# Optimization experiments

Hardware: AMD Instinct MI355X
Metric: run time of the kernel (lower is better)

The kernel has to match this reference:

```python
import jax, jax.numpy as jnp
import numpy as np

N = 20000      # nodes
E = 160000     # edges
F_IN = 128     # num_node_features
D = 128        # embedding_size (out_channels)
H = 4          # heads
NEG = 0.2      # GATv2Conv negative_slope
N_LAYERS = 3


def setup_inputs() -> dict:
    key = jax.random.key(0)
    ks = jax.random.split(key, 12)
    s = 0.05
    return {
        "x": jax.random.normal(ks[0], (N, F_IN), jnp.float32),
        "edge_index": jax.random.randint(ks[1], (2, E), 0, N, jnp.int64),
        "edge_attr": jax.random.normal(ks[2], (E, 2), jnp.float32),
        "Wf": jax.random.normal(ks[3], (F_IN, D), jnp.float32) * s,
        "bf": jnp.zeros((D,), jnp.float32),
        "Wl": jax.random.normal(ks[4], (D, H * D), jnp.float32) * s,
        "bl": jnp.zeros((H * D,), jnp.float32),
        "Wr": jax.random.normal(ks[5], (D, H * D), jnp.float32) * s,
        "br": jnp.zeros((H * D,), jnp.float32),
        "We": jax.random.normal(ks[6], (2, H * D), jnp.float32) * s,
        "att": jax.random.normal(ks[7], (H, D), jnp.float32) * s,
        "bias_out": jnp.zeros((D,), jnp.float32),
    }


def reference(x, edge_index, edge_attr, Wf, bf, Wl, bl, Wr, br, We, att, bias_out):
    src, dst = edge_index[0], edge_index[1]

    # add_self_loops with fill_value='mean': self-loop edge_attr = mean of
    # incoming edge_attr per node (0 where a node has no incoming edges)
    ea_sum = jax.ops.segment_sum(edge_attr, dst, num_segments=N)            # [N,2]
    cnt = jax.ops.segment_sum(jnp.ones((E,), edge_attr.dtype), dst, num_segments=N)
    loop_attr = ea_sum / jnp.maximum(cnt, 1.0)[:, None]
    loop_idx = jnp.arange(N, dtype=src.dtype)
    fsrc = jnp.concatenate([src, loop_idx])                                  # [E+N]
    fdst = jnp.concatenate([dst, loop_idx])
    fea = jnp.concatenate([edge_attr, loop_attr], axis=0)                    # [E+N,2]

    ee = (fea @ We).reshape(-1, H, D)                                        # [E+N,H,D]

    def gatv2_layer(h):
        xl = (h @ Wl + bl).reshape(N, H, D)   # lin_l -> source-side / message
        xr = (h @ Wr + br).reshape(N, H, D)   # lin_r -> target-side
        e = jax.nn.leaky_relu(xl[fsrc] + xr[fdst] + ee, NEG)                 # [E+N,H,D]
        logits = jnp.einsum('ehd,hd->eh', e, att)                            # [E+N,H]
        m = jax.ops.segment_max(logits, fdst, num_segments=N)                # [N,H]
        w = jnp.exp(logits - m[fdst])
        denom = jax.ops.segment_sum(w, fdst, num_segments=N)                 # [N,H]
        alpha = w / denom[fdst]                                              # segment softmax
        msg = xl[fsrc] * alpha[..., None]                                    # [E+N,H,D]
        out = jax.ops.segment_sum(msg, fdst, num_segments=N)                 # [N,H,D]
        return out.mean(axis=1) + bias_out                                   # concat=False

    h = x @ Wf + bf
    for _ in range(N_LAYERS):
        h = jax.nn.leaky_relu(gatv2_layer(h), 0.01)  # F.leaky_relu default slope
    return h
```

## Files before the change

kernel.cpp:

```cpp
#include <hip/hip_runtime.h>
#include <hip/hip_bf16.h>

#define NN 20000
#define NE 160000
#define EF (NE + NN)
#define DD 128
#define HH 4
#define NPA (NN * DD)
#define NPW (1024 * 128 + 128 * 128 + 1024)
#define DEGB ((NE + 255) / 256)
#define NBLK 40

typedef unsigned short u16;
typedef unsigned int u32;

using short8  = __attribute__((ext_vector_type(8))) short;
using ushort8 = __attribute__((ext_vector_type(8))) unsigned short;
using float4v = __attribute__((ext_vector_type(4))) float;
using f32x2   = __attribute__((ext_vector_type(2))) float;

__device__ __forceinline__ float bf2f(u16 u) {
    union { u32 i; float f; } c;
    c.i = ((u32)u) << 16;
    return c.f;
}
__device__ __forceinline__ u16 f2bf(float f) {
    union { float f; u32 u; } c;
    c.f = f;
    u32 u = c.u;
    u32 r = (u + 0x7fffu + ((u >> 16) & 1u)) >> 16;
    return (u16)r;
}

template<int CTRL>
__device__ __forceinline__ float dpp_add(float v) {
    int t = __builtin_amdgcn_update_dpp(0, __builtin_bit_cast(int, v),
                                        CTRL, 0xf, 0xf, true);
    return v + __builtin_bit_cast(float, t);
}


__global__ void k_zero_i(int* __restrict__ p, int n) {
    int i = blockIdx.x * blockDim.x + threadIdx.x;
    if (i < n) p[i] = 0;
}

__global__ void k_zero_f(float* __restrict__ p, int n) {
    int i = blockIdx.x * blockDim.x + threadIdx.x;
    if (i < n) p[i] = 0.f;
}


__global__ void k_degpack(const int* __restrict__ ei, const float* __restrict__ ea,
                          const float* __restrict__ x,
                          const float* __restrict__ Wl, const float* __restrict__ Wr,
                          const float* __restrict__ bl, const float* __restrict__ br,
                          const float* __restrict__ Wf,
                          int* __restrict__ cnt, float* __restrict__ ea_sum,
                          u16* __restrict__ Axh, u16* __restrict__ Axl,
                          u16* __restrict__ W2Th, u16* __restrict__ W2Tl,
                          u16* __restrict__ WfTh, u16* __restrict__ WfTl,
                          float* __restrict__ bias2) {
    int gb = blockIdx.x;
    if (gb < DEGB) {
        int e = gb * 256 + threadIdx.x;
        if (e >= NE) return;
        int t = ei[NE + e];
        atomicAdd(&cnt[t], 1);
        atomicAdd(&ea_sum[t * 2 + 0], ea[e * 2 + 0]);
        atomicAdd(&ea_sum[t * 2 + 1], ea[e * 2 + 1]);
        return;
    }
    int i = (gb - DEGB) * 256 + threadIdx.x;
    if (i < NPA) {
        float a = x[i];
        u16 h = f2bf(a);
        Axh[i] = h;
        Axl[i] = f2bf(a - bf2f(h));
        return;
    }
    i -= NPA;
    if (i < 1024 * 128) {
        int n = i >> 7, k = i & 127;
        float w = (n < 512) ? Wl[k * 512 + n] : Wr[k * 512 + (n - 512)];
        u16 h = f2bf(w);
        W2Th[n * 128 + k] = h;
        W2Tl[n * 128 + k] = f2bf(w - bf2f(h));
    } else if (i < 1024 * 128 + 128 * 128) {
        int u = i - 1024 * 128;
        int n = u >> 7, k = u & 127;
        float w = Wf[k * 128 + n];
        u16 h = f2bf(w);
        WfTh[n * 128 + k] = h;
        WfTl[n * 128 + k] = f2bf(w - bf2f(h));
    } else if (i < NPW) {
        int n = i - (1024 * 128 + 128 * 128);
        bias2[n] = (n < 512) ? bl[n] : br[n - 512];
    }
}


__global__ __launch_bounds__(512) void k_scan_a(const int* __restrict__ cnt,
                                                int* __restrict__ rowptr,
                                                int* __restrict__ bsum) {
    __shared__ int ws[8];
    int tid = threadIdx.x;
    int i = blockIdx.x * 512 + tid;
    int l = tid & 63, w = tid >> 6;
    int v = (i < NN) ? (cnt[i] + 1) : 0;
    #pragma unroll
    for (int off = 1; off < 64; off <<= 1) {
        int u = __shfl_up(v, off, 64);
        if (l >= off) v += u;
    }
    if (l == 63) ws[w] = v;
    __syncthreads();
    if (w == 0) {
        int s = (l < 8) ? ws[l] : 0;
        #pragma unroll
        for (int off = 1; off < 8; off <<= 1) {
            int u = __shfl_up(s, off, 64);
            if (l >= off) s += u;
        }
        if (l < 8) ws[l] = s;
    }
    __syncthreads();
    v += (w > 0) ? ws[w - 1] : 0;
    if (i < NN) rowptr[i + 1] = v;
    if (tid == 511) bsum[blockIdx.x] = v;
}

__global__ void k_scan_c(int* __restrict__ rowptr, const int* __restrict__ bsum) {
    int l = threadIdx.x & 63;
    int v = (l < NBLK) ? bsum[l] : 0;
    #pragma unroll
    for (int off = 1; off < 64; off <<= 1) {
        int u = __shfl_up(v, off, 64);
        if (l >= off) v += u;
    }
    int i = blockIdx.x * blockDim.x + threadIdx.x;
    int j = i >> 9;
    int off = (j > 0) ? __shfl(v, j - 1, 64) : 0;
    if (i < NN) rowptr[i + 1] += off;
    if (i == 0) rowptr[0] = 0;
}


__global__ void k_fill(const int* __restrict__ ei, const float* __restrict__ ea,
                       const int* __restrict__ rowptr, int* __restrict__ fillc,
                       const int* __restrict__ cnt, const float* __restrict__ ea_sum,
                       int* __restrict__ srcs,
                       float* __restrict__ fa0, float* __restrict__ fa1) {
    int e = blockIdx.x * blockDim.x + threadIdx.x;
    if (e < NE) {
        int s = ei[e], t = ei[NE + e];
        int pos = atomicAdd(&fillc[t], 1);
        int slot = rowptr[t] + pos;
        srcs[slot] = s;
        fa0[slot] = ea[e * 2];
        fa1[slot] = ea[e * 2 + 1];
    } else if (e < NE + NN) {
        int n = e - NE;
        int slot = rowptr[n + 1] - 1;
        srcs[slot] = n;
        float c = fmaxf((float)cnt[n], 1.f);
        fa0[slot] = ea_sum[n * 2 + 0] / c;
        fa1[slot] = ea_sum[n * 2 + 1] / c;
    }
}


template<int SPLIT, int NB>
__global__ __launch_bounds__(256, 3) void k_mgemm(
        const u16* __restrict__ Ahg, const u16* __restrict__ Alg,
        const u16* __restrict__ BTh, const u16* __restrict__ BTl,
        const float* __restrict__ bias, float* __restrict__ C1,
        u16* __restrict__ C2b,
        u16* __restrict__ Oh, u16* __restrict__ Ol, int M) {
    __shared__ u16 sAh[64 * 128], sBh[64 * 128], sBl[64 * 128];
    int m0 = blockIdx.y * 64;
    int t = threadIdx.x;
    int lane = t & 63;
    int wm = (t >> 6) & 1;
    int wn = t >> 7;
    int fm = lane & 15;
    int q8 = (lane >> 4) * 8;

    short8 fal[4][2];
    #pragma unroll
    for (int i = 0; i < 2; ++i) {
        const u16* p = Alg + (size_t)(m0 + wm * 32 + i * 16 + fm) * 128 + q8;
        #pragma unroll
        for (int kk = 0; kk < 4; ++kk)
            fal[kk][i] = *(const short8*)(p + kk * 32);
    }

    #pragma unroll
    for (int i = 0; i < 4; ++i) {
        int c = t + 256 * i;
        int row = c >> 4, ch = c & 15;
        int gm = m0 + row;
        short8 va = {0, 0, 0, 0, 0, 0, 0, 0};
        if (gm < M) va = *(const short8*)&Ahg[gm * 128 + ch * 8];
        *(short8*)&sAh[row * 128 + ((ch ^ (row & 15)) << 3)] = va;
    }

    int cq = q8 >> 3;

    for (int bb = 0; bb < NB; ++bb) {
        int n0 = (blockIdx.x * NB + bb) * 64;
        __syncthreads();
        #pragma unroll
        for (int i = 0; i < 4; ++i) {
            int c = t + 256 * i;
            int row = c >> 4, ch = c & 15;
            int gn = n0 + row;
            int d = row * 128 + ((ch ^ (row & 15)) << 3);
            *(short8*)&sBh[d] = *(const short8*)&BTh[gn * 128 + ch * 8];
            *(short8*)&sBl[d] = *(const short8*)&BTl[gn * 128 + ch * 8];
        }
        __syncthreads();

        float4v zz = {0.f, 0.f, 0.f, 0.f};
        float4v acc[2][2];
        acc[0][0] = zz; acc[0][1] = zz; acc[1][0] = zz; acc[1][1] = zz;

        #pragma unroll
        for (int k0 = 0; k0 < 128; k0 += 32) {
            int cl = (k0 >> 3) + cq;
            int sw = (cl ^ fm) << 3;
            short8 fah[2], fbh[2], fbl[2];
            #pragma unroll
            for (int i = 0; i < 2; ++i) {
                int mr = wm * 32 + i * 16 + fm;
                fah[i] = *(const short8*)&sAh[mr * 128 + sw];
                int nr = wn * 32 + i * 16 + fm;
                fbh[i] = *(const short8*)&sBh[nr * 128 + sw];
                fbl[i] = *(const short8*)&sBl[nr * 128 + sw];
            }
            #pragma unroll
            for (int i = 0; i < 2; ++i)
                #pragma unroll
                for (int j = 0; j < 2; ++j) {
                    acc[i][j] = __builtin_amdgcn_mfma_f32_16x16x32_bf16(fah[i], fbh[j], acc[i][j], 0, 0, 0);
                    acc[i][j] = __builtin_amdgcn_mfma_f32_16x16x32_bf16(fah[i], fbl[j], acc[i][j], 0, 0, 0);
                    acc[i][j] = __builtin_amdgcn_mfma_f32_16x16x32_bf16(fal[k0 >> 5][i], fbh[j], acc[i][j], 0, 0, 0);
                }
        }

        #pragma unroll
        for (int i = 0; i < 2; ++i) {
            #pragma unroll
            for (int j = 0; j < 2; ++j) {
                int gn = n0 + wn * 32 + j * 16 + fm;
                float bv = bias[gn];
                #pragma unroll
                for (int r = 0; r < 4; ++r) {
                    int gm = m0 + wm * 32 + i * 16 + (lane >> 4) * 4 + r;
                    if (gm < M) {
                        float v = acc[i][j][r] + bv;
                        if (SPLIT) {
                            u16 h = f2bf(v);
                            Oh[gm * 128 + gn] = h;
                            Ol[gm * 128 + gn] = f2bf(v - bf2f(h));
                        } else if (n0 < 512) {
                            C1[gm * 512 + gn] = v;
                        } else {
                            C2b[gm * 512 + gn - 512] = f2bf(v);
                        }
                    }
                }
            }
        }
    }
}


__global__ __launch_bounds__(256) void k_gat(
        const int* __restrict__ rowptr, const int* __restrict__ srcs,
        const float* __restrict__ fa0, const float* __restrict__ fa1,
        const float* __restrict__ xl, const u16* __restrict__ xr,
        const float* __restrict__ We, const float* __restrict__ att,
        const float* __restrict__ bias_out,
        u16* __restrict__ Oh, u16* __restrict__ Ol,
        float* __restrict__ outp, int last) {
    __shared__ float sacc[2][512];
    __shared__ float sden[2][4];
    int wv = threadIdx.x >> 6;
    int pair = wv >> 1;
    int half = wv & 1;
    int n = blockIdx.x * 2 + pair;
    int l = threadIdx.x & 63;
    int d0 = l * 8;

    f32x2 xr2[4], we0p[4], we1p[4], at6p[4], at4p[4];
    {
        ushort8 u = *reinterpret_cast<const ushort8*>(&xr[(size_t)n * 512 + d0]);
        #pragma unroll
        for (int k = 0; k < 4; ++k) {
            f32x2 t; t.x = bf2f(u[2 * k]); t.y = bf2f(u[2 * k + 1]);
            xr2[k] = t;
        }
        const f32x2* w0 = reinterpret_cast<const f32x2*>(&We[d0]);
        const f32x2* w1 = reinterpret_cast<const f32x2*>(&We[512 + d0]);
        const f32x2* av = reinterpret_cast<const f32x2*>(&att[d0]);
        #pragma unroll
        for (int k = 0; k < 4; ++k) {
            we0p[k] = w0[k];
            we1p[k] = w1[k];
            f32x2 a = av[k];
            at6p[k] = a * 0.6f;
            at4p[k] = a * 0.4f;
        }
    }

    int b0 = rowptr[n], b1 = rowptr[n + 1];
    int nit = (b1 - b0 - half + 1) >> 1;

    int sv = 0, f0i = 0, f1i = 0;
    {
        int me = b0 + half + 2 * l;
        if (l < nit) {
            sv  = srcs[me];
            f0i = __builtin_bit_cast(int, fa0[me]);
            f1i = __builtin_bit_cast(int, fa1[me]);
        }
    }

    f32x2 acc2[4];
    acc2[0] = f32x2{0.f, 0.f}; acc2[1] = f32x2{0.f, 0.f};
    acc2[2] = f32x2{0.f, 0.f}; acc2[3] = f32x2{0.f, 0.f};
    float den = 0.f;

    auto body = [&](float4 A, float4 B, float f0, float f1) {
        f32x2 f0p; f0p.x = f0; f0p.y = f0;
        f32x2 f1p; f1p.x = f1; f1p.y = f1;
        f32x2 xv2[4];
        xv2[0].x = A.x; xv2[0].y = A.y;
        xv2[1].x = A.z; xv2[1].y = A.w;
        xv2[2].x = B.x; xv2[2].y = B.y;
        xv2[3].x = B.z; xv2[3].y = B.w;
        f32x2 p2 = {0.f, 0.f};
        #pragma unroll
        for (int k = 0; k < 4; ++k) {
            f32x2 t = __builtin_elementwise_fma(f0p, we0p[k], xr2[k]);
            t = __builtin_elementwise_fma(f1p, we1p[k], t);
            f32x2 v2 = xv2[k] + t;
            f32x2 a2 = __builtin_elementwise_abs(v2);
            p2 = __builtin_elementwise_fma(at6p[k], v2, p2);
            p2 = __builtin_elementwise_fma(at4p[k], a2, p2);
        }
        float p = p2.x + p2.y;
        p = dpp_add<0xB1>(p);
        p = dpp_add<0x4E>(p);
        p = dpp_add<0x124>(p);
        p = dpp_add<0x128>(p);
        float wt = __expf(p);
        den += wt;
        f32x2 wtp; wtp.x = wt; wtp.y = wt;
        #pragma unroll
        for (int k = 0; k < 4; ++k)
            acc2[k] = __builtin_elementwise_fma(wtp, xv2[k], acc2[k]);
    };

    int nfast = nit < 64 ? nit : 64;
    #pragma unroll 2
    for (int it = 0; it < nfast; ++it) {
        int   s  = __builtin_amdgcn_readlane(sv, it);
        float f0 = __builtin_bit_cast(float, __builtin_amdgcn_readlane(f0i, it));
        float f1 = __builtin_bit_cast(float, __builtin_amdgcn_readlane(f1i, it));
        const float* xp = &xl[(size_t)s * 512 + d0];
        float4 A = *reinterpret_cast<const float4*>(xp);
        float4 B = *reinterpret_cast<const float4*>(xp + 4);
        body(A, B, f0, f1);
    }
    for (int e = b0 + half + 128; e < b1; e += 2) {
        int s = srcs[e];
        const float* xp = &xl[(size_t)s * 512 + d0];
        float4 A = *reinterpret_cast<const float4*>(xp);
        float4 B = *reinterpret_cast<const float4*>(xp + 4);
        body(A, B, fa0[e], fa1[e]);
    }

    if (half == 1) {
        *reinterpret_cast<float4*>(&sacc[pair][d0]) =
            make_float4(acc2[0].x, acc2[0].y, acc2[1].x, acc2[1].y);
        *reinterpret_cast<float4*>(&sacc[pair][d0 + 4]) =
            make_float4(acc2[2].x, acc2[2].y, acc2[3].x, acc2[3].y);
        if ((l & 15) == 0) sden[pair][l >> 4] = den;
    }
    __syncthreads();
    if (half == 1) return;
    float acc[8] = {acc2[0].x, acc2[0].y, acc2[1].x, acc2[1].y,
                    acc2[2].x, acc2[2].y, acc2[3].x, acc2[3].y};
    #pragma unroll
    for (int k = 0; k < 8; ++k) acc[k] += sacc[pair][d0 + k];
    den += sden[pair][l >> 4];
    float inv = 1.f / den;
    float val[8];
    #pragma unroll
    for (int k = 0; k < 8; ++k) {
        float v = acc[k] * inv;
        v += __shfl_xor(v, 16, 64);
        v += __shfl_xor(v, 32, 64);
        val[k] = v;
    }
    if (l < 16) {
        #pragma unroll
        for (int k = 0; k < 8; ++k) {
            float v = val[k] * 0.25f + bias_out[d0 + k];
            v = v > 0.f ? v : 0.01f * v;
            val[k] = v;
        }
        if (last) {
            #pragma unroll
            for (int k = 0; k < 8; ++k) outp[n * 128 + d0 + k] = val[k];
        } else {
            #pragma unroll
            for (int k = 0; k < 8; ++k) {
                u16 hv = f2bf(val[k]);
                Oh[n * 128 + d0 + k] = hv;
                Ol[n * 128 + d0 + k] = f2bf(val[k] - bf2f(hv));
            }
        }
    }
}


extern "C" void kernel_launch(void* const* d_in, const int* in_sizes, int n_in,
                              void* d_out, int out_size, void* d_ws, size_t ws_size,
                              hipStream_t stream) {
    size_t o = 0;
    auto alloc = [&](size_t bytes) { size_t cur = o; o += (bytes + 255) & ~(size_t)255; return cur; };
    size_t off_cnt    = alloc((size_t)NN * 4);
    size_t off_fillc  = alloc((size_t)NN * 4);
    size_t off_easum  = alloc((size_t)NN * 2 * 4);
    size_t off_rowptr = alloc((size_t)(NN + 1) * 4);
    size_t off_bsum   = alloc((size_t)NBLK * 4);
    size_t off_srcs   = alloc((size_t)EF * 4);
    size_t off_fa0    = alloc((size_t)EF * 4);
    size_t off_fa1    = alloc((size_t)EF * 4);
    size_t off_axh    = alloc((size_t)NN * DD * 2);
    size_t off_axl    = alloc((size_t)NN * DD * 2);
    size_t off_ah     = alloc((size_t)NN * DD * 2);
    size_t off_al     = alloc((size_t)NN * DD * 2);
    size_t off_xl     = alloc((size_t)NN * 512 * 4);
    size_t off_xr     = alloc((size_t)NN * 512 * 2);
    size_t off_w2th   = alloc((size_t)1024 * 128 * 2);
    size_t off_w2tl   = alloc((size_t)1024 * 128 * 2);
    size_t off_wfth   = alloc((size_t)128 * 128 * 2);
    size_t off_wftl   = alloc((size_t)128 * 128 * 2);
    size_t off_bias2  = alloc((size_t)1024 * 4);
    size_t need = o;

    bool ok = (n_in == 12) && d_ws != nullptr && ws_size >= need
           && out_size == NN * DD
           && in_sizes[0] == NN * DD && in_sizes[1] == 2 * NE
           && in_sizes[2] == NE * 2 && in_sizes[3] == 128 * 128
           && in_sizes[5] == 128 * 512 && in_sizes[9] == 2 * 512
           && in_sizes[10] == 4 * 128 && in_sizes[11] == 128;
    if (!ok) {
        k_zero_f<<<(NN * DD + 255) / 256, 256, 0, stream>>>((float*)d_out, NN * DD);
        return;
    }

    const float* x        = (const float*)d_in[0];
    const int*   ei       = (const int*)d_in[1];
    const float* ea       = (const float*)d_in[2];
    const float* Wf       = (const float*)d_in[3];
    const float* bf       = (const float*)d_in[4];
    const float* Wl       = (const float*)d_in[5];
    const float* bl       = (const float*)d_in[6];
    const float* Wr       = (const float*)d_in[7];
    const float* br       = (const float*)d_in[8];
    const float* We       = (const float*)d_in[9];
    const float* att      = (const float*)d_in[10];
    const float* bias_out = (const float*)d_in[11];

    char* base = (char*)d_ws;
    int*   cnt    = (int*)(base + off_cnt);
    int*   fillc  = (int*)(base + off_fillc);
    float* ea_sum = (float*)(base + off_easum);
    int*   rowptr = (int*)(base + off_rowptr);
    int*   bsum   = (int*)(base + off_bsum);
    int*   srcs   = (int*)(base + off_srcs);
    float* fa0    = (float*)(base + off_fa0);
    float* fa1    = (float*)(base + off_fa1);
    u16*   Axh    = (u16*)(base + off_axh);
    u16*   Axl    = (u16*)(base + off_axl);
    u16*   Ah     = (u16*)(base + off_ah);
    u16*   Al     = (u16*)(base + off_al);
    float* xl     = (float*)(base + off_xl);
    u16*   xr     = (u16*)(base + off_xr);
    u16*   W2Th   = (u16*)(base + off_w2th);
    u16*   W2Tl   = (u16*)(base + off_w2tl);
    u16*   WfTh   = (u16*)(base + off_wfth);
    u16*   WfTl   = (u16*)(base + off_wftl);
    float* bias2  = (float*)(base + off_bias2);

    int zero_ints = (int)((off_easum + (size_t)NN * 2 * 4 - off_cnt) / 4);
    k_zero_i<<<(zero_ints + 255) / 256, 256, 0, stream>>>(cnt, zero_ints);

    int packb = (NPA + NPW + 255) / 256;
    k_degpack<<<DEGB + packb, 256, 0, stream>>>(ei, ea, x, Wl, Wr, bl, br, Wf,
                                                cnt, ea_sum, Axh, Axl,
                                                W2Th, W2Tl, WfTh, WfTl, bias2);
    k_scan_a<<<NBLK, 512, 0, stream>>>(cnt, rowptr, bsum);
    k_scan_c<<<(NN + 255) / 256, 256, 0, stream>>>(rowptr, bsum);
    k_fill<<<(NE + NN + 255) / 256, 256, 0, stream>>>(ei, ea, rowptr, fillc,
                                                      cnt, ea_sum, srcs, fa0, fa1);

    const int MT = (NN + 63) / 64;
    k_mgemm<1, 2><<<dim3(1, MT), 256, 0, stream>>>(Axh, Axl, WfTh, WfTl,
                                                   bf, nullptr, nullptr, Ah, Al, NN);

    for (int layer = 0; layer < 3; ++layer) {
        k_mgemm<0, 8><<<dim3(2, MT), 256, 0, stream>>>(Ah, Al, W2Th, W2Tl,
                                                       bias2, xl, xr, nullptr, nullptr, NN);
        int last = (layer == 2);
        k_gat<<<NN / 2, 256, 0, stream>>>(rowptr, srcs, fa0, fa1, xl, xr,
                                          We, att, bias_out, Ah, Al,
                                          (float*)d_out, last);
    }
}
```

Baseline: 405.3 us.

## Use direct global-to-LDS loads in GEMM, one node per GAT block, memset zeroing

The GEMM tile loads now use global_load_lds to copy A and B tiles straight into shared memory, keeping the XOR swizzle by permuting the global addresses. Out-of-range A rows are clamped to the last valid row instead of being zero-filled. The GAT kernel now runs one node per 128-thread block instead of two nodes per 256-thread block, so a block no longer waits on its slower node, and its fast loop is unrolled 4x. The custom zero kernel is replaced with hipMemsetAsync. Risks include the clamped garbage rows in the last tile and more blocks with less work each for the GAT launch.

```diff
diff --git a/kernel.cpp b/kernel.cpp
--- a/kernel.cpp
+++ b/kernel.cpp
@@ -39,11 +39,13 @@
     return v + __builtin_bit_cast(float, t);
 }
 
-
-__global__ void k_zero_i(int* __restrict__ p, int n) {
-    int i = blockIdx.x * blockDim.x + threadIdx.x;
-    if (i < n) p[i] = 0;
-}
+__device__ __forceinline__ void gld16(const void* g, void* l) {
+    __builtin_amdgcn_global_load_lds(
+        (const __attribute__((address_space(1))) unsigned int*)g,
+        (__attribute__((address_space(3))) unsigned int*)l,
+        16, 0, 0);
+}
+
 
 __global__ void k_zero_f(float* __restrict__ p, int n) {
     int i = blockIdx.x * blockDim.x + threadIdx.x;
@@ -197,12 +199,12 @@
 
     #pragma unroll
     for (int i = 0; i < 4; ++i) {
-        int c = t + 256 * i;
+        int cb = (t & 192) + 256 * i;
+        int c = cb + lane;
         int row = c >> 4, ch = c & 15;
         int gm = m0 + row;
-        short8 va = {0, 0, 0, 0, 0, 0, 0, 0};
-        if (gm < M) va = *(const short8*)&Ahg[gm * 128 + ch * 8];
-        *(short8*)&sAh[row * 128 + ((ch ^ (row & 15)) << 3)] = va;
+        if (gm >= M) gm = M - 1;
+        gld16(&Ahg[(size_t)gm * 128 + ((ch ^ (row & 15)) << 3)], &sAh[cb * 8]);
     }
 
     int cq = q8 >> 3;
@@ -212,12 +214,12 @@
         __syncthreads();
         #pragma unroll
         for (int i = 0; i < 4; ++i) {
-            int c = t + 256 * i;
+            int cb = (t & 192) + 256 * i;
+            int c = cb + lane;
             int row = c >> 4, ch = c & 15;
-            int gn = n0 + row;
-            int d = row * 128 + ((ch ^ (row & 15)) << 3);
-            *(short8*)&sBh[d] = *(const short8*)&BTh[gn * 128 + ch * 8];
-            *(short8*)&sBl[d] = *(const short8*)&BTl[gn * 128 + ch * 8];
+            size_t gofs = (size_t)(n0 + row) * 128 + ((ch ^ (row & 15)) << 3);
+            gld16(&BTh[gofs], &sBh[cb * 8]);
+            gld16(&BTl[gofs], &sBl[cb * 8]);
         }
         __syncthreads();
 
@@ -276,7 +278,7 @@
 }
 
 
-__global__ __launch_bounds__(256) void k_gat(
+__global__ __launch_bounds__(128) void k_gat(
         const int* __restrict__ rowptr, const int* __restrict__ srcs,
         const float* __restrict__ fa0, const float* __restrict__ fa1,
         const float* __restrict__ xl, const u16* __restrict__ xr,
@@ -284,12 +286,10 @@
         const float* __restrict__ bias_out,
         u16* __restrict__ Oh, u16* __restrict__ Ol,
         float* __restrict__ outp, int last) {
-    __shared__ float sacc[2][512];
-    __shared__ float sden[2][4];
-    int wv = threadIdx.x >> 6;
-    int pair = wv >> 1;
-    int half = wv & 1;
-    int n = blockIdx.x * 2 + pair;
+    __shared__ float sacc[512];
+    __shared__ float sden[4];
+    int half = threadIdx.x >> 6;
+    int n = blockIdx.x;
     int l = threadIdx.x & 63;
     int d0 = l * 8;
 
@@ -364,7 +364,7 @@
     };
 
     int nfast = nit < 64 ? nit : 64;
-    #pragma unroll 2
+    #pragma unroll 4
     for (int it = 0; it < nfast; ++it) {
         int   s  = __builtin_amdgcn_readlane(sv, it);
         float f0 = __builtin_bit_cast(float, __builtin_amdgcn_readlane(f0i, it));
@@ -383,19 +383,19 @@
     }
 
     if (half == 1) {
-        *reinterpret_cast<float4*>(&sacc[pair][d0]) =
+        *reinterpret_cast<float4*>(&sacc[d0]) =
             make_float4(acc2[0].x, acc2[0].y, acc2[1].x, acc2[1].y);
-        *reinterpret_cast<float4*>(&sacc[pair][d0 + 4]) =
+        *reinterpret_cast<float4*>(&sacc[d0 + 4]) =
             make_float4(acc2[2].x, acc2[2].y, acc2[3].x, acc2[3].y);
-        if ((l & 15) == 0) sden[pair][l >> 4] = den;
+        if ((l & 15) == 0) sden[l >> 4] = den;
     }
     __syncthreads();
     if (half == 1) return;
     float acc[8] = {acc2[0].x, acc2[0].y, acc2[1].x, acc2[1].y,
                     acc2[2].x, acc2[2].y, acc2[3].x, acc2[3].y};
     #pragma unroll
-    for (int k = 0; k < 8; ++k) acc[k] += sacc[pair][d0 + k];
-    den += sden[pair][l >> 4];
+    for (int k = 0; k < 8; ++k) acc[k] += sacc[d0 + k];
+    den += sden[l >> 4];
     float inv = 1.f / den;
     float val[8];
     #pragma unroll
@@ -498,8 +498,8 @@
     u16*   WfTl   = (u16*)(base + off_wftl);
     float* bias2  = (float*)(base + off_bias2);
 
-    int zero_ints = (int)((off_easum + (size_t)NN * 2 * 4 - off_cnt) / 4);
-    k_zero_i<<<(zero_ints + 255) / 256, 256, 0, stream>>>(cnt, zero_ints);
+    size_t zero_bytes = off_easum + (size_t)NN * 2 * 4 - off_cnt;
+    hipMemsetAsync(cnt, 0, zero_bytes, stream);
 
     int packb = (NPA + NPW + 255) / 256;
     k_degpack<<<DEGB + packb, 256, 0, stream>>>(ei, ea, x, Wl, Wr, bl, br, Wf,
@@ -518,8 +518,8 @@
         k_mgemm<0, 8><<<dim3(2, MT), 256, 0, stream>>>(Ah, Al, W2Th, W2Tl,
                                                        bias2, xl, xr, nullptr, nullptr, NN);
         int last = (layer == 2);
-        k_gat<<<NN / 2, 256, 0, stream>>>(rowptr, srcs, fa0, fa1, xl, xr,
-                                          We, att, bias_out, Ah, Al,
-                                          (float*)d_out, last);
-    }
-}
+        k_gat<<<NN, 128, 0, stream>>>(rowptr, srcs, fa0, fa1, xl, xr,
+                                      We, att, bias_out, Ah, Al,
+                                      (float*)d_out, last);
+    }
+}
```

Measured after the change: 396.4 us. 2.2% less time.
